# Kernel tuning notes

Hardware: AMD Instinct MI355X
Metric: run time of the kernel (lower is better)

## Reference

```python
import jax, jax.numpy as jnp
import numpy as np

EPS = 1e-5  # torch BatchNorm2d default eps

def _bn_train(x, g, b):
    # BatchNorm2d in training mode: batch statistics over (N, H, W), biased variance
    m = x.mean(axis=(0, 2, 3), keepdims=True)
    v = x.var(axis=(0, 2, 3), keepdims=True)
    return g[None, :, None, None] * (x - m) / jnp.sqrt(v + EPS) + b[None, :, None, None]

def _conv3(x, w, b):
    y = jax.lax.conv_general_dilated(x, w, (1, 1), 'SAME',
                                     dimension_numbers=('NCHW', 'OIHW', 'NCHW'))
    return y + b[None, :, None, None]

def _conv1(x, w, b):
    # 1x1 conv == per-pixel matmul; w: [out, in]
    return jnp.einsum('bchw,oc->bohw', x, w) + b[None, :, None, None]

def _projector(x, w1, b1, g1, be1, w2, b2, g2, be2):
    h = jax.nn.relu(_bn_train(_conv3(x, w1, b1), g1, be1))
    return _bn_train(_conv1(h, w2, b2), g2, be2)

def _cross_teacher_attention(s, teachers, wq, bq, wk, bk, wv, bv):
    B, C, H, W = s.shape
    scale = C ** -0.5
    q = _conv1(s, wq, bq).reshape(B, C, H * W).transpose(0, 2, 1)  # [B, HW, C]
    outs, ws = [], []
    for t in teachers:  # small fixed list of teachers (structural branch)
        k = _conv1(t, wk, bk).reshape(B, C, H * W).transpose(0, 2, 1)
        v = _conv1(t, wv, bv).reshape(B, C, H * W).transpose(0, 2, 1)
        a = jax.nn.softmax(jnp.einsum('bqc,bkc->bqk', q, k) * scale, axis=-1)  # [B, HW, HW]
        outs.append(jnp.einsum('bqk,bkc->bqc', a, v))                          # [B, HW, C]
        ws.append(a.mean(axis=-1))                                             # [B, HW]
    w = jax.nn.softmax(jnp.stack(ws, axis=-1), axis=-1)          # [B, HW, T]
    fused = jnp.einsum('bqt,tbqc->bqc', w, jnp.stack(outs, 0))   # weighted sum over teachers
    fused = fused.reshape(B, H, W, C).transpose(0, 3, 1, 2)      # [B, C, H, W]
    return s + fused

def setup_inputs() -> dict:
    key = jax.random.key(0)
    ks = jax.random.split(key, 16)
    B, C, H, W = 8, 128, 56, 56
    T = 256  # teacher projector output dim
    d = {}
    d['student_mid'] = jax.random.normal(ks[0], (B, C, H, W), jnp.float32)
    d['t1_mid'] = jax.random.normal(ks[1], (B, C, H, W), jnp.float32)
    d['t2_mid'] = jax.random.normal(ks[2], (B, C, H, W), jnp.float32)
    for i, n in enumerate(['q', 'k', 'v']):
        d['w' + n] = jax.random.normal(ks[3 + i], (C, C), jnp.float32) * 0.05
        d['b' + n] = jnp.zeros((C,), jnp.float32)
    for p, off in (('p1', 6), ('p2', 10)):
        d[p + '_w1'] = jax.random.normal(ks[off], (C, C, 3, 3), jnp.float32) * 0.05
        d[p + '_b1'] = jnp.zeros((C,), jnp.float32)
        d[p + '_g1'] = jnp.ones((C,), jnp.float32)
        d[p + '_be1'] = jnp.zeros((C,), jnp.float32)
        d[p + '_w2'] = jax.random.normal(ks[off + 1], (T, C), jnp.float32) * 0.05
        d[p + '_b2'] = jnp.zeros((T,), jnp.float32)
        d[p + '_g2'] = jnp.ones((T,), jnp.float32)
        d[p + '_be2'] = jnp.zeros((T,), jnp.float32)
    return d

def reference(student_mid, t1_mid, t2_mid, wq, bq, wk, bk, wv, bv,
              p1_w1, p1_b1, p1_g1, p1_be1, p1_w2, p1_b2, p1_g2, p1_be2,
              p2_w1, p2_b1, p2_g1, p2_be1, p2_w2, p2_b2, p2_g2, p2_be2):
    # Per-teacher projectors: computed by the torch module but their outputs are
    # never consumed by the attention (s_feat_proj is unused) -> dead code.
    _sp1 = _projector(student_mid, p1_w1, p1_b1, p1_g1, p1_be1, p1_w2, p1_b2, p1_g2, p1_be2)
    _sp2 = _projector(student_mid, p2_w1, p2_b1, p2_g1, p2_be1, p2_w2, p2_b2, p2_g2, p2_be2)
    del _sp1, _sp2
    return _cross_teacher_attention(student_mid, [t1_mid, t2_mid], wq, bq, wk, bk, wv, bv)
```

## Files before the change

### kernel.cpp

```cpp
#include <hip/hip_runtime.h>

#define HW 3136
#define NB 8
#define CD 128
#define NT (HW/64)
#define QSCALE 0.12751750206f

typedef __attribute__((ext_vector_type(8))) short short8;
typedef __attribute__((ext_vector_type(4))) short short4v;
typedef __attribute__((ext_vector_type(4))) float floatx4;
typedef __attribute__((ext_vector_type(4))) unsigned short ushort4v;

static __device__ __forceinline__ unsigned short f2b(float f){
  union { float f; unsigned u; } v; v.f = f;
  unsigned r = v.u + 0x7FFFu + ((v.u >> 16) & 1u);
  return (unsigned short)(r >> 16);
}
static __device__ __forceinline__ float b2f(unsigned short h){
  union { unsigned u; float f; } v; v.u = ((unsigned)h) << 16;
  return v.f;
}
static __device__ __forceinline__ unsigned cvtpk(float lo, float hi){
  unsigned r;
  asm("v_cvt_pk_bf16_f32 %0, %1, %2" : "=v"(r) : "v"(lo), "v"(hi));
  return r;
}

#if __has_builtin(__builtin_amdgcn_mfma_f32_16x16x16bf16_1k)
#define MFMA16(a,b,c) __builtin_amdgcn_mfma_f32_16x16x16bf16_1k(a,b,c,0,0,0)
#elif __has_builtin(__builtin_amdgcn_mfma_f32_16x16x16_bf16)
#define MFMA16(a,b,c) __builtin_amdgcn_mfma_f32_16x16x16_bf16(a,b,c,0,0,0)
#else
static __device__ __forceinline__ floatx4 mfma16_asm(short4v a, short4v b, floatx4 c){
  floatx4 d;
  asm volatile("v_mfma_f32_16x16x16_bf16 %0, %1, %2, %3\n\ts_nop 7\n\ts_nop 7"
               : "=v"(d) : "v"(a), "v"(b), "v"(c));
  return d;
}
#define MFMA16(a,b,c) mfma16_asm(a,b,c)
#endif

__global__ __launch_bounds__(256) void proj_kernel(
    const float* __restrict__ s, const float* __restrict__ t1, const float* __restrict__ t2,
    const float* __restrict__ wq, const float* __restrict__ bq,
    const float* __restrict__ wk, const float* __restrict__ bk,
    const float* __restrict__ wv, const float* __restrict__ bv,
    unsigned short* __restrict__ qkv)
{
  __shared__ __align__(16) unsigned short WL[CD][136];
  __shared__ __align__(16) unsigned short xsT[64][136];
  const int job = blockIdx.z;
  const float* x; const float* w; const float* bias; float scl; int cmajor; size_t dstoff;
  switch(job){
    case 0: x=s;  w=wq; bias=bq; scl=QSCALE; cmajor=0; dstoff=0; break;
    case 1: x=t1; w=wk; bias=bk; scl=1.f;    cmajor=0; dstoff=1; break;
    case 2: x=t1; w=wv; bias=bv; scl=1.f;    cmajor=1; dstoff=2; break;
    case 3: x=t2; w=wk; bias=bk; scl=1.f;    cmajor=0; dstoff=3; break;
    default:x=t2; w=wv; bias=bv; scl=1.f;    cmajor=1; dstoff=4; break;
  }
  const size_t TS = (size_t)NB*HW*CD;
  const int b   = blockIdx.y;
  const int hw0 = blockIdx.x * 64;
  const int tid = threadIdx.x;

  for (int i = 0; i < 16; i++){
    int flat = tid + i*256;
    int o = flat >> 5, cq = (flat & 31)*4;
    floatx4 wv4 = *(const floatx4*)(w + (size_t)o*CD + cq);
    ushort4v pk;
    for (int j=0;j<4;j++) pk[j] = f2b(wv4[j]);
    *(ushort4v*)&WL[o][cq] = pk;
  }
  const float* xb = x + (size_t)b*CD*HW + hw0;
  for (int i = 0; i < 8; i++){
    int flat = (tid + i*256)*4;
    int c = flat >> 6, hh = flat & 63;
    floatx4 xv = *(const floatx4*)(xb + (size_t)c*HW + hh);
    for (int j=0;j<4;j++) xsT[hh+j][c] = f2b(xv[j]);
  }
  __syncthreads();

  const int m = tid & 15, quad = (tid >> 4) & 3, wv_ = tid >> 6;
  short8 af[4];
#pragma unroll
  for (int dk=0;dk<4;dk++)
    af[dk] = *(const short8*)&xsT[wv_*16 + m][dk*32 + quad*8];

  unsigned short* dstK = qkv + dstoff*TS + ((size_t)b*HW + hw0)*CD;
  unsigned short* dstV = qkv + dstoff*TS + (size_t)b*CD*HW;
  if (!cmajor){
#pragma unroll
    for (int nt=0;nt<8;nt++){
      floatx4 acc = *(const floatx4*)(bias + nt*16 + quad*4);
#pragma unroll
      for (int dk=0;dk<4;dk++){
        short8 bf = *(const short8*)&WL[nt*16 + m][dk*32 + quad*8];
        acc = __builtin_amdgcn_mfma_f32_16x16x32_bf16(bf, af[dk], acc, 0,0,0);
      }
      ushort4v pk;
      for (int r=0;r<4;r++) pk[r] = f2b(acc[r]*scl);
      *(ushort4v*)&dstK[(size_t)(wv_*16 + m)*CD + nt*16 + quad*4] = pk;
    }
  } else {
    float bb[8];
#pragma unroll
    for (int nt=0;nt<8;nt++) bb[nt] = bias[nt*16 + m];
#pragma unroll
    for (int nt=0;nt<8;nt++){
      floatx4 acc = {bb[nt],bb[nt],bb[nt],bb[nt]};
#pragma unroll
      for (int dk=0;dk<4;dk++){
        short8 bf = *(const short8*)&WL[nt*16 + m][dk*32 + quad*8];
        acc = __builtin_amdgcn_mfma_f32_16x16x32_bf16(af[dk], bf, acc, 0,0,0);
      }
      ushort4v pk;
      for (int r=0;r<4;r++) pk[r] = f2b(acc[r]*scl);
      *(ushort4v*)&dstV[(size_t)(nt*16 + m)*HW + hw0 + wv_*16 + quad*4] = pk;
    }
  }
}

__global__ __launch_bounds__(256,2) void attn_kernel(
    const unsigned short* __restrict__ qkv,
    unsigned short* __restrict__ Og)
{
  __shared__ __align__(16) unsigned short smem[32768 + 512 + 128];
  float* lrb  = (float*)(smem + 32768);
  float* invL = (float*)(smem + 32768 + 512);

  const int l  = blockIdx.x;
  const int b  = l & 7;
  const int qt = l >> 3;
  const size_t TS = (size_t)NB*HW*CD;
  const unsigned short* Q = qkv + (size_t)b*HW*CD;

  const int tid  = threadIdx.x;
  const int wv_  = tid >> 6;
  const int lane = tid & 63;
  const int m    = lane & 15;
  const int quad = lane >> 4;
  const int q0   = qt*64;

  unsigned koff[4];
  {
    const int kr_ = lane >> 4, kc_ = lane & 15;
#pragma unroll
    for (int i=0;i<4;i++){
      const int krow = wv_*16 + i*4 + kr_;
      koff[i] = (unsigned)(krow*CD + ((kc_ ^ ((i*4 + kr_) & 7))*8));
    }
  }
  const int      vrow0 = wv_*32 + (lane>>3);
  const unsigned vcs   = (unsigned)(((lane&7) ^ (lane>>3))*8);

  short8 qf[4][4];
#pragma unroll
  for (int qs=0;qs<4;qs++){
    const unsigned short* qr = Q + (size_t)(q0 + qs*16 + m)*CD + quad*8;
#pragma unroll
    for (int dk=0;dk<4;dk++) qf[qs][dk] = *(const short8*)(qr + dk*32);
  }

#define STAGE(buf, ktile) do { \
    const unsigned short* kt_src = K + (size_t)(ktile)*64*CD; \
    const unsigned short* vt_src = V + (size_t)(ktile)*64; \
    unsigned short* kl = (unsigned short*)smem + (buf)*16384 + wv_*2048; \
    unsigned short* vl = (unsigned short*)smem + (buf)*16384 + 8192 + wv_*2048; \
    _Pragma("unroll") \
    for (int i_=0;i_<4;i_++) \
      __builtin_amdgcn_global_load_lds( \
        (const __attribute__((address_space(1))) void*)(kt_src + koff[i_]), \
        (__attribute__((address_space(3))) void*)(kl + i_*512), 16, 0, 0); \
    _Pragma("unroll") \
    for (int i_=0;i_<4;i_++) \
      __builtin_amdgcn_global_load_lds( \
        (const __attribute__((address_space(1))) void*)(vt_src + (size_t)(vrow0 + i_*8)*HW + vcs), \
        (__attribute__((address_space(3))) void*)(vl + i_*512), 16, 0, 0); \
  } while(0)

  for (int t2=0; t2<2; t2++){
    const unsigned short* K = qkv + TS*(size_t)(1 + 2*t2) + (size_t)b*HW*CD;
    const unsigned short* V = qkv + TS*(size_t)(2 + 2*t2) + (size_t)b*CD*HW;

    floatx4 Oc[8][4];
#pragma unroll
    for (int i=0;i<8;i++)
#pragma unroll
      for (int j=0;j<4;j++) Oc[i][j] = (floatx4)0.f;
    float lr[4] = {0.f,0.f,0.f,0.f};

    STAGE(0, 0);

    for (int kt = 0; kt < NT; kt++){
      const int cur = kt & 1;
      __builtin_amdgcn_s_barrier();
      if (kt < NT-1){
        STAGE(cur^1, kt+1);
        asm volatile("s_waitcnt vmcnt(8)" ::: "memory");
      } else {
        asm volatile("s_waitcnt vmcnt(0)" ::: "memory");
      }
      __builtin_amdgcn_sched_barrier(0);
      __builtin_amdgcn_s_barrier();
      asm volatile("" ::: "memory");

      const unsigned short* Kc = (const unsigned short*)smem + cur*16384;
      const unsigned short* Vc = (const unsigned short*)smem + cur*16384 + 8192;

      short8 af[4];
#pragma unroll
      for (int dk=0;dk<4;dk++)
        af[dk] = *(const short8*)&Kc[(wv_*16 + m)*128 + (((dk*4 + quad) ^ (m & 7))*8)];

      short4v pfv[4];
#pragma unroll
      for (int qs=0;qs<4;qs++){
        floatx4 acc = (floatx4)0.f;
        __builtin_amdgcn_s_setprio(1);
#pragma unroll
        for (int dk=0;dk<4;dk++)
          acc = __builtin_amdgcn_mfma_f32_16x16x32_bf16(af[dk], qf[qs][dk], acc, 0,0,0);
        __builtin_amdgcn_s_setprio(0);
        float c0 = __builtin_amdgcn_exp2f(acc[0]);
        float c1 = __builtin_amdgcn_exp2f(acc[1]);
        float c2 = __builtin_amdgcn_exp2f(acc[2]);
        float c3 = __builtin_amdgcn_exp2f(acc[3]);
        lr[qs] += (c0 + c1) + (c2 + c3);
        union { unsigned u[2]; short4v s; } pk;
        pk.u[0] = cvtpk(c0, c1);
        pk.u[1] = cvtpk(c2, c3);
        pfv[qs] = pk.s;
      }

      __builtin_amdgcn_s_setprio(1);
#pragma unroll
      for (int ct=0;ct<8;ct++){
        short4v vf = *(const short4v*)&Vc[(ct*16 + m)*64 +
                       (((2*wv_ + (quad>>1)) ^ (m & 7))*8) + (quad&1)*4];
#pragma unroll
        for (int qs=0;qs<4;qs++)
          Oc[ct][qs] = MFMA16(vf, pfv[qs], Oc[ct][qs]);
      }
      __builtin_amdgcn_s_setprio(0);
    }

#pragma unroll
    for (int qs=0;qs<4;qs++){
      lr[qs] += __shfl_xor(lr[qs], 16, 64);
      lr[qs] += __shfl_xor(lr[qs], 32, 64);
    }
    if (quad == 0){
#pragma unroll
      for (int qs=0;qs<4;qs++) lrb[wv_*64 + qs*16 + m] = lr[qs];
    }
    __syncthreads();
    if (tid < 64)
      invL[tid] = 1.f/(lrb[tid] + lrb[64+tid] + lrb[128+tid] + lrb[192+tid]);
    __syncthreads();

    float* Of = (float*)smem;
    unsigned short* ob = Og + ((size_t)t2*NB + b)*HW*CD + (size_t)q0*CD;
    const int qlr = wv_*16 + (lane>>2);
    const int c8  = (lane&3)*8;
#pragma unroll
    for (int rd=0; rd<4; rd++){
#pragma unroll
      for (int cc=0; cc<2; cc++){
#pragma unroll
        for (int qs=0; qs<4; qs++)
          *(floatx4*)&Of[wv_*2304 + (qs*16+m)*36 + cc*16 + quad*4] = Oc[rd*2+cc][qs];
      }
      __syncthreads();
      floatx4 s0 = (floatx4)0.f, s1 = (floatx4)0.f;
#pragma unroll
      for (int w=0; w<4; w++){
        s0 += *(const floatx4*)&Of[w*2304 + qlr*36 + c8];
        s1 += *(const floatx4*)&Of[w*2304 + qlr*36 + c8 + 4];
      }
      float iv = invL[qlr];
      short8 o;
#pragma unroll
      for (int j=0;j<4;j++){
        o[j]   = (short)f2b(s0[j]*iv);
        o[4+j] = (short)f2b(s1[j]*iv);
      }
      *(short8*)&ob[(size_t)qlr*CD + rd*32 + c8] = o;
      __syncthreads();
    }
  }
#undef STAGE
}

__global__ __launch_bounds__(256) void combine_kernel(
    const float* __restrict__ s, const unsigned short* __restrict__ Og,
    float* __restrict__ out)
{
  __shared__ __align__(16) float T[32][132];
  const int b   = blockIdx.y;
  const int hw0 = blockIdx.x * 32;
  const int tid = threadIdx.x;
  const unsigned short* O1 = Og + ((size_t)b*HW + hw0)*CD;
  const unsigned short* O2 = O1 + (size_t)NB*HW*CD;
  for (int i=0;i<2;i++){
    int flat = tid + i*256;
    int row = flat >> 4, col0 = (flat & 15)*8;
    short8 a  = *(const short8*)(O1 + (size_t)row*CD + col0);
    short8 c2 = *(const short8*)(O2 + (size_t)row*CD + col0);
    floatx4 v0, v1;
#pragma unroll
    for (int j=0;j<4;j++){
      v0[j] = 0.5f*(b2f((unsigned short)a[j])   + b2f((unsigned short)c2[j]));
      v1[j] = 0.5f*(b2f((unsigned short)a[4+j]) + b2f((unsigned short)c2[4+j]));
    }
    *(floatx4*)&T[row][col0]   = v0;
    *(floatx4*)&T[row][col0+4] = v1;
  }
  __syncthreads();
  const int c  = tid >> 1;
  const int h0 = (tid & 1)*16;
  const float* sr = s   + ((size_t)b*CD + c)*HW + hw0 + h0;
  float*     orow = out + ((size_t)b*CD + c)*HW + hw0 + h0;
  for (int j0=0;j0<16;j0+=4){
    floatx4 sv = *(const floatx4*)(sr + j0);
    floatx4 ov;
    for (int jj=0;jj<4;jj++) ov[jj] = sv[jj] + T[h0+j0+jj][c];
    *(floatx4*)(orow + j0) = ov;
  }
}

extern "C" void kernel_launch(void* const* d_in, const int* in_sizes, int n_in,
                              void* d_out, int out_size, void* d_ws, size_t ws_size,
                              hipStream_t stream)
{
  const float* s  = (const float*)d_in[0];
  const float* t1 = (const float*)d_in[1];
  const float* t2 = (const float*)d_in[2];
  const float* wq = (const float*)d_in[3];
  const float* bq = (const float*)d_in[4];
  const float* wk = (const float*)d_in[5];
  const float* bk = (const float*)d_in[6];
  const float* wv = (const float*)d_in[7];
  const float* bv = (const float*)d_in[8];
  float* out = (float*)d_out;

  unsigned short* qkv = (unsigned short*)d_ws;
  unsigned short* Og  = qkv + (size_t)5*NB*HW*CD;

  hipLaunchKernelGGL(proj_kernel,    dim3(49,8,5), dim3(256), 0, stream,
                     s,t1,t2,wq,bq,wk,bk,wv,bv,qkv);
  hipLaunchKernelGGL(attn_kernel,    dim3(392),    dim3(256), 0, stream, qkv, Og);
  hipLaunchKernelGGL(combine_kernel, dim3(98,8),   dim3(256), 0, stream, s, Og, out);
}
```

Baseline: 275.9 us.

## Pre-convert QKV weights to bf16 once and load projection operands directly from global

Adds a small kernel that converts the q/k/v weight matrices to bf16 once per call, so each projection block no longer converts the full fp32 weight into shared memory. The projection kernel drops shared memory and the barrier entirely: each lane gathers its x fragment straight from global with strided loads and packs it with v_cvt_pk_bf16, and reads weight fragments directly from the bf16 global copy. This adds a kernel launch and uncoalesced strided x reads, relying on L2 for weight reuse, in exchange for removing the LDS staging and sync overhead.

After: 296.1 us. 1.07x slower.

```diff
diff --git a/kernel.cpp b/kernel.cpp
--- a/kernel.cpp
+++ b/kernel.cpp
@@ -40,82 +40,92 @@
 #define MFMA16(a,b,c) mfma16_asm(a,b,c)
 #endif
 
+__global__ __launch_bounds__(256) void wconv_kernel(
+    const float* __restrict__ wq, const float* __restrict__ wk,
+    const float* __restrict__ wv, unsigned short* __restrict__ Wb)
+{
+  const float* src = blockIdx.x==0 ? wq : (blockIdx.x==1 ? wk : wv);
+  unsigned short* dst = Wb + (size_t)blockIdx.x*CD*CD;
+  for (int i = threadIdx.x; i < CD*CD/8; i += 256){
+    floatx4 v0 = *(const floatx4*)(src + (size_t)i*8);
+    floatx4 v1 = *(const floatx4*)(src + (size_t)i*8 + 4);
+    union { unsigned u[4]; ushort4v p[2]; } pk;
+    pk.u[0] = cvtpk(v0[0], v0[1]);
+    pk.u[1] = cvtpk(v0[2], v0[3]);
+    pk.u[2] = cvtpk(v1[0], v1[1]);
+    pk.u[3] = cvtpk(v1[2], v1[3]);
+    *(ushort4v*)(dst + (size_t)i*8)     = pk.p[0];
+    *(ushort4v*)(dst + (size_t)i*8 + 4) = pk.p[1];
+  }
+}
+
 __global__ __launch_bounds__(256) void proj_kernel(
     const float* __restrict__ s, const float* __restrict__ t1, const float* __restrict__ t2,
-    const float* __restrict__ wq, const float* __restrict__ bq,
-    const float* __restrict__ wk, const float* __restrict__ bk,
-    const float* __restrict__ wv, const float* __restrict__ bv,
+    const float* __restrict__ bq, const float* __restrict__ bk, const float* __restrict__ bv,
+    const unsigned short* __restrict__ Wb,
     unsigned short* __restrict__ qkv)
 {
-  __shared__ __align__(16) unsigned short WL[CD][136];
-  __shared__ __align__(16) unsigned short xsT[64][136];
   const int job = blockIdx.z;
-  const float* x; const float* w; const float* bias; float scl; int cmajor; size_t dstoff;
+  const float* x; const float* bias; float scl; int cmajor; size_t dstoff; int wsel;
   switch(job){
-    case 0: x=s;  w=wq; bias=bq; scl=QSCALE; cmajor=0; dstoff=0; break;
-    case 1: x=t1; w=wk; bias=bk; scl=1.f;    cmajor=0; dstoff=1; break;
-    case 2: x=t1; w=wv; bias=bv; scl=1.f;    cmajor=1; dstoff=2; break;
-    case 3: x=t2; w=wk; bias=bk; scl=1.f;    cmajor=0; dstoff=3; break;
-    default:x=t2; w=wv; bias=bv; scl=1.f;    cmajor=1; dstoff=4; break;
+    case 0: x=s;  wsel=0; bias=bq; scl=QSCALE; cmajor=0; dstoff=0; break;
+    case 1: x=t1; wsel=1; bias=bk; scl=1.f;    cmajor=0; dstoff=1; break;
+    case 2: x=t1; wsel=2; bias=bv; scl=1.f;    cmajor=1; dstoff=2; break;
+    case 3: x=t2; wsel=1; bias=bk; scl=1.f;    cmajor=0; dstoff=3; break;
+    default:x=t2; wsel=2; bias=bv; scl=1.f;    cmajor=1; dstoff=4; break;
   }
   const size_t TS = (size_t)NB*HW*CD;
   const int b   = blockIdx.y;
   const int hw0 = blockIdx.x * 64;
   const int tid = threadIdx.x;
-
-  for (int i = 0; i < 16; i++){
-    int flat = tid + i*256;
-    int o = flat >> 5, cq = (flat & 31)*4;
-    floatx4 wv4 = *(const floatx4*)(w + (size_t)o*CD + cq);
-    ushort4v pk;
-    for (int j=0;j<4;j++) pk[j] = f2b(wv4[j]);
-    *(ushort4v*)&WL[o][cq] = pk;
-  }
-  const float* xb = x + (size_t)b*CD*HW + hw0;
-  for (int i = 0; i < 8; i++){
-    int flat = (tid + i*256)*4;
-    int c = flat >> 6, hh = flat & 63;
-    floatx4 xv = *(const floatx4*)(xb + (size_t)c*HW + hh);
-    for (int j=0;j<4;j++) xsT[hh+j][c] = f2b(xv[j]);
-  }
-  __syncthreads();
-
   const int m = tid & 15, quad = (tid >> 4) & 3, wv_ = tid >> 6;
-  short8 af[4];
-#pragma unroll
-  for (int dk=0;dk<4;dk++)
-    af[dk] = *(const short8*)&xsT[wv_*16 + m][dk*32 + quad*8];
-
-  unsigned short* dstK = qkv + dstoff*TS + ((size_t)b*HW + hw0)*CD;
-  unsigned short* dstV = qkv + dstoff*TS + (size_t)b*CD*HW;
+  const int hw = hw0 + wv_*16 + m;
+
+  const float* xb = x + (size_t)b*CD*HW + (size_t)quad*8*HW + hw;
+  short8 xf[4];
+#pragma unroll
+  for (int dk=0;dk<4;dk++){
+    union { unsigned u[4]; short8 s8; } p;
+#pragma unroll
+    for (int w=0;w<4;w++){
+      float v0 = xb[(size_t)(dk*32 + 2*w    )*HW];
+      float v1 = xb[(size_t)(dk*32 + 2*w + 1)*HW];
+      p.u[w] = cvtpk(v0, v1);
+    }
+    xf[dk] = p.s8;
+  }
+
+  const unsigned short* W = Wb + (size_t)wsel*CD*CD;
   if (!cmajor){
+    unsigned short* dstK = qkv + dstoff*TS + (size_t)b*HW*CD;
 #pragma unroll
     for (int nt=0;nt<8;nt++){
       floatx4 acc = *(const floatx4*)(bias + nt*16 + quad*4);
 #pragma unroll
       for (int dk=0;dk<4;dk++){
-        short8 bf = *(const short8*)&WL[nt*16 + m][dk*32 + quad*8];
-        acc = __builtin_amdgcn_mfma_f32_16x16x32_bf16(bf, af[dk], acc, 0,0,0);
-      }
-      ushort4v pk;
-      for (int r=0;r<4;r++) pk[r] = f2b(acc[r]*scl);
-      *(ushort4v*)&dstK[(size_t)(wv_*16 + m)*CD + nt*16 + quad*4] = pk;
+        short8 wf = *(const short8*)&W[(size_t)(nt*16 + m)*CD + dk*32 + quad*8];
+        acc = __builtin_amdgcn_mfma_f32_16x16x32_bf16(wf, xf[dk], acc, 0,0,0);
+      }
+      union { unsigned u[2]; ushort4v p; } pk;
+      pk.u[0] = cvtpk(acc[0]*scl, acc[1]*scl);
+      pk.u[1] = cvtpk(acc[2]*scl, acc[3]*scl);
+      *(ushort4v*)&dstK[(size_t)hw*CD + nt*16 + quad*4] = pk.p;
     }
   } else {
-    float bb[8];
-#pragma unroll
-    for (int nt=0;nt<8;nt++) bb[nt] = bias[nt*16 + m];
+    unsigned short* dstV = qkv + dstoff*TS + (size_t)b*CD*HW;
 #pragma unroll
     for (int nt=0;nt<8;nt++){
-      floatx4 acc = {bb[nt],bb[nt],bb[nt],bb[nt]};
+      float bb = bias[nt*16 + m];
+      floatx4 acc = {bb,bb,bb,bb};
 #pragma unroll
       for (int dk=0;dk<4;dk++){
-        short8 bf = *(const short8*)&WL[nt*16 + m][dk*32 + quad*8];
-        acc = __builtin_amdgcn_mfma_f32_16x16x32_bf16(af[dk], bf, acc, 0,0,0);
-      }
-      ushort4v pk;
-      for (int r=0;r<4;r++) pk[r] = f2b(acc[r]*scl);
-      *(ushort4v*)&dstV[(size_t)(nt*16 + m)*HW + hw0 + wv_*16 + quad*4] = pk;
+        short8 wf = *(const short8*)&W[(size_t)(nt*16 + m)*CD + dk*32 + quad*8];
+        acc = __builtin_amdgcn_mfma_f32_16x16x32_bf16(xf[dk], wf, acc, 0,0,0);
+      }
+      union { unsigned u[2]; ushort4v p; } pk;
+      pk.u[0] = cvtpk(acc[0], acc[1]);
+      pk.u[1] = cvtpk(acc[2], acc[3]);
+      *(ushort4v*)&dstV[(size_t)(nt*16 + m)*HW + hw0 + wv_*16 + quad*4] = pk.p;
     }
   }
 }
@@ -345,9 +355,11 @@
 
   unsigned short* qkv = (unsigned short*)d_ws;
   unsigned short* Og  = qkv + (size_t)5*NB*HW*CD;
-
+  unsigned short* Wb  = Og  + (size_t)2*NB*HW*CD;
+
+  hipLaunchKernelGGL(wconv_kernel,   dim3(3),      dim3(256), 0, stream, wq, wk, wv, Wb);
   hipLaunchKernelGGL(proj_kernel,    dim3(49,8,5), dim3(256), 0, stream,
-                     s,t1,t2,wq,bq,wk,bk,wv,bv,qkv);
+                     s, t1, t2, bq, bk, bv, Wb, qkv);
   hipLaunchKernelGGL(attn_kernel,    dim3(392),    dim3(256), 0, stream, qkv, Og);
   hipLaunchKernelGGL(combine_kernel, dim3(98,8),   dim3(256), 0, stream, s, Og, out);
 }
```
